# Optimization experiments

Measured on AMD Instinct MI355X. Metric: run time of the kernel, lower is better.

## Reference

```python
import jax, jax.numpy as jnp
import numpy as np

B, P, G, CIN, COUT, WD, K3 = 4, 32768, 64, 128, 128, 512, 27
N = B * P


def _build_kernel_map(rng):
    # random sparse occupancy per batch instance on a G^3 grid
    flat = np.stack([rng.choice(G ** 3, size=P, replace=False) for _ in range(B)])  # [B,P]
    b = np.repeat(np.arange(B), P).astype(np.int64)
    f = flat.reshape(-1).astype(np.int64)
    x = f // (G * G); y = (f // G) % G; z = f % G
    keys = b * (G ** 3) + f
    order = np.argsort(keys); skeys = keys[order]
    offsets = [(dx, dy, dz) for dx in (-1, 0, 1) for dy in (-1, 0, 1) for dz in (-1, 0, 1)]
    in_idx = np.full((K3, N), N, np.int32)   # N is a dummy (zero-feature) row
    out_idx = np.full((K3, N), N, np.int32)  # N is a dummy (discarded) output row
    for k, (dx, dy, dz) in enumerate(offsets):
        nx, ny, nz = x + dx, y + dy, z + dz
        inb = (nx >= 0) & (nx < G) & (ny >= 0) & (ny < G) & (nz >= 0) & (nz < G)
        nkey = b * (G ** 3) + (nx * G + ny) * G + nz
        pos = np.clip(np.searchsorted(skeys, nkey), 0, N - 1)
        found = inb & (skeys[pos] == nkey)
        cnt = int(found.sum())
        in_idx[k, :cnt] = order[pos[found]]
        out_idx[k, :cnt] = np.nonzero(found)[0]
    return b.astype(np.int32), in_idx, out_idx


def setup_inputs() -> dict:
    rng = np.random.default_rng(0)
    batch_idx, in_idx, out_idx = _build_kernel_map(rng)
    key = jax.random.key(0)
    k1, k2, k3, k4 = jax.random.split(key, 4)
    return {
        "x_feat": jax.random.normal(k1, (N, CIN), jnp.float32),
        "w": jax.random.normal(k2, (B, WD), jnp.float32),
        "affine_weight": jax.random.normal(k3, (CIN, WD), jnp.float32),
        "affine_bias": jnp.ones((CIN,), jnp.float32),  # bias_init=1
        "conv_weight": jax.random.normal(k4, (COUT, CIN, 3, 3, 3), jnp.float32),
        "conv_bias": jnp.zeros((COUT,), jnp.float32),
        "magnitude_ema": jnp.ones((), jnp.float32),
        "batch_idx": jnp.asarray(batch_idx),
        "in_idx": jnp.asarray(in_idx),
        "out_idx": jnp.asarray(out_idx),
    }


def reference(x_feat, w, affine_weight, affine_bias, conv_weight, conv_bias,
              magnitude_ema, batch_idx, in_idx, out_idx):
    n, cin = x_feat.shape
    cout = conv_weight.shape[0]
    # affine: FullyConnectedLayer with weight_gain = 1/sqrt(in_features), bias_init=1
    styles = w @ (affine_weight * (1.0 / np.sqrt(affine_weight.shape[1]))).T + affine_bias  # [B,Cin]
    # demodulate pre-normalization
    wn = conv_weight * jax.lax.rsqrt(jnp.mean(jnp.square(conv_weight), axis=(1, 2, 3, 4), keepdims=True))
    sn = styles * jax.lax.rsqrt(jnp.mean(jnp.square(styles)))
    sw = wn[None] * sn[:, None, :, None, None, None]              # [B,Cout,Cin,3,3,3]
    dcoefs = jax.lax.rsqrt(jnp.sum(jnp.square(sw), axis=(2, 3, 4, 5)) + 1e-8)  # [B,Cout]
    # non-fused modconv: per-point style modulation (index_select by batch column)
    xmod = x_feat * sn[batch_idx]                                 # [N,Cin]
    xpad = jnp.concatenate([xmod, jnp.zeros((1, cin), xmod.dtype)], axis=0)
    # sparse conv: gather -> GEMM -> scatter-add per kernel offset
    wk = jnp.transpose(wn.reshape(cout, cin, K3), (2, 1, 0))      # [27,Cin,Cout]
    out = jnp.zeros((n + 1, cout), x_feat.dtype)
    for k in range(K3):
        out = out.at[out_idx[k]].add(xpad[in_idx[k]] @ wk[k])
    out = out[:n]
    out = out * dcoefs[batch_idx]                                 # demodulation per point
    out = out * jax.lax.rsqrt(magnitude_ema)                      # input_gain
    # fused bias + leaky relu + gain + clamp
    out = out + conv_bias
    out = jnp.where(out < 0, 0.2 * out, out) * np.sqrt(2.0)
    return jnp.clip(out, -256.0, 256.0)
```

## Files before the change

### kernel.cpp

```cpp
#include <hip/hip_runtime.h>
#include <stdint.h>

#define NPTS 131072
#define CINC 128
#define COUTC 128
#define WDIM 512
#define K3 27

typedef float f32x4 __attribute__((ext_vector_type(4)));
typedef __bf16 bf16x8 __attribute__((ext_vector_type(8)));

#define GLOAD_LDS16(g, l) \
  __builtin_amdgcn_global_load_lds((const __attribute__((address_space(1))) void*)(g), \
                                   (__attribute__((address_space(3))) void*)(l), 16, 0, 0)

__device__ __forceinline__ unsigned short f2bf(float x){
  union { float f; uint32_t u; } v; v.f = x;
  uint32_t u = v.u;
  uint32_t r = (u + 0x7fffu + ((u >> 16) & 1u)) >> 16;
  return (unsigned short)r;
}

__global__ void k_styles_dot(const float* __restrict__ w, const float* __restrict__ aw,
                             const float* __restrict__ ab, float* __restrict__ styles){
  int wave = threadIdx.x >> 6, lane = threadIdx.x & 63;
  int blk = blockIdx.x * 4 + wave;
  int b = blk >> 7, c = blk & 127;
  const float4* wr = (const float4*)(w + b * WDIM);
  const float4* ar = (const float4*)(aw + c * WDIM);
  float4 w0 = wr[lane * 2], w1 = wr[lane * 2 + 1];
  float4 a0 = ar[lane * 2], a1 = ar[lane * 2 + 1];
  float s = w0.x * a0.x + w0.y * a0.y + w0.z * a0.z + w0.w * a0.w
          + w1.x * a1.x + w1.y * a1.y + w1.z * a1.z + w1.w * a1.w;
  for (int off = 32; off > 0; off >>= 1) s += __shfl_down(s, off, 64);
  if (lane == 0) styles[blk] = s * 0.04419417382415922f + ab[c];
}

__global__ void k_sn_dco(const float* __restrict__ styles, const float* __restrict__ vmat,
                         const float* __restrict__ wnorm, const float* __restrict__ mag,
                         float* __restrict__ sn, float* __restrict__ dco2){
  __shared__ float red[512];
  int t = threadIdx.x;
  float s = styles[t];
  red[t] = s * s;
  __syncthreads();
  for (int off = 256; off > 0; off >>= 1){
    if (t < off) red[t] += red[t + off];
    __syncthreads();
  }
  float rs = rsqrtf(red[0] * (1.0f / 512.0f));
  if (blockIdx.x == 0) sn[t] = s * rs;
  int wave = t >> 6, lane = t & 63;
  int pair = blockIdx.x * 8 + wave;
  int b = pair >> 7, co = pair & 127;
  float s0 = styles[b * 128 + lane] * rs, s1 = styles[b * 128 + 64 + lane] * rs;
  float sum = vmat[co * 128 + lane] * s0 * s0 + vmat[co * 128 + 64 + lane] * s1 * s1;
  for (int off = 32; off > 0; off >>= 1) sum += __shfl_down(sum, off, 64);
  if (lane == 0){
    float wn = wnorm[co];
    dco2[pair] = rsqrtf(sum * wn * wn + 1e-8f) * rsqrtf(mag[0]);
  }
}

__global__ void k_prep_w(const float* __restrict__ cw, float* __restrict__ wnorm,
                         float* __restrict__ vmat, unsigned short* __restrict__ bpack){
  __shared__ float red[128];
  int co = blockIdx.x, cin = threadIdx.x;
  const float* p = cw + co * 3456 + cin * 27;
  float r[27];
  float v = 0.f;
  #pragma unroll
  for (int k = 0; k < 27; k++){ r[k] = p[k]; v += r[k] * r[k]; }
  vmat[co * 128 + cin] = v;
  red[cin] = v;
  __syncthreads();
  for (int off = 64; off > 0; off >>= 1){
    if (cin < off) red[cin] += red[cin + off];
    __syncthreads();
  }
  float wn_s = rsqrtf(red[0] * (1.0f / 3456.0f));
  if (cin == 0) wnorm[co] = wn_s;
  int grp = co >> 4, m = co & 15;
  int kk = cin >> 5, q = (cin >> 3) & 3, j = cin & 7;
  #pragma unroll
  for (int k = 0; k < 27; k++){
    int idx = ((k * 32 + kk * 8 + grp) * 64 + q * 16 + m) * 8 + j;
    bpack[idx] = f2bf(r[k] * wn_s);
  }
}

__global__ void k_xmod(const float* __restrict__ x, const float* __restrict__ sn,
                       const int* __restrict__ bidx, unsigned short* __restrict__ xpad){
  int gid = blockIdx.x * 256 + threadIdx.x;
  const int total = (NPTS + 1) * 32;
  if (gid >= total) return;
  int n = gid >> 5;
  int c4 = (gid & 31) * 4;
  unsigned short o0, o1, o2, o3;
  if (n < NPTS){
    int b = bidx[n];
    float4 xv = *(const float4*)(x + (size_t)n * CINC + c4);
    float4 sv = *(const float4*)(sn + b * CINC + c4);
    o0 = f2bf(xv.x * sv.x); o1 = f2bf(xv.y * sv.y);
    o2 = f2bf(xv.z * sv.z); o3 = f2bf(xv.w * sv.w);
  } else { o0 = o1 = o2 = o3 = 0; }
  *(ushort4*)(xpad + (size_t)n * CINC + c4) = make_ushort4(o0, o1, o2, o3);
}

__global__ void k_invinit(int* __restrict__ invT){
  int j = blockIdx.x * 256 + threadIdx.x;
  int k = blockIdx.y;
  invT[k * NPTS + j] = NPTS;
}

__global__ void k_invscat(const int* __restrict__ out_idx, const int* __restrict__ in_idx,
                          int* __restrict__ invT){
  int j = blockIdx.x * 256 + threadIdx.x;
  int k = blockIdx.y;
  int o = out_idx[k * NPTS + j];
  if (o < NPTS) invT[k * NPTS + o] = in_idx[k * NPTS + j];
}

__global__ __launch_bounds__(256, 4) void k_conv(
    const unsigned short* __restrict__ xpad,
    const unsigned short* __restrict__ bpack,
    const int* __restrict__ invT,
    const float* __restrict__ dco2,
    const float* __restrict__ cbias,
    const int* __restrict__ bidx,
    float* __restrict__ out){
  __shared__ __align__(16) unsigned short Ash[2 * 64 * 128];
  int t = threadIdx.x;
  int wave = t >> 6, lane = t & 63;
  int wm = wave >> 1, wn = wave & 1;
  int q = lane >> 4, m16 = lane & 15;
  int base_pt = blockIdx.x * 64;

  f32x4 acc[2][4];
  #pragma unroll
  for (int i = 0; i < 2; i++)
    #pragma unroll
    for (int j = 0; j < 4; j++) acc[i][j] = (f32x4){0.f, 0.f, 0.f, 0.f};

  auto prefetch = [&](int k, int bufsel){
    const int* invk = invT + k * NPTS + base_pt;
    unsigned short* Ab = Ash + bufsel * (64 * 128);
    #pragma unroll
    for (int i = 0; i < 4; i++){
      int chunk = i * 256 + t;
      int row = chunk >> 4, c = chunk & 15;
      int inv = invk[row];
      const unsigned short* src = xpad + (size_t)inv * CINC + ((c ^ row) & 15) * 8;
      GLOAD_LDS16(src, Ab + chunk * 8);
    }
  };

  prefetch(0, 0);
  for (int k = 0; k < K3; k++){
    __syncthreads();
    if (k + 1 < K3) prefetch(k + 1, (k + 1) & 1);
    const unsigned short* Ab = Ash + (k & 1) * (64 * 128);
    const unsigned short* Bg = bpack + k * 16384;
    #pragma unroll
    for (int kk = 0; kk < 4; kk++){
      int cA = ((kk * 4 + q) ^ m16) & 15;
      bf16x8 a0 = *(const bf16x8*)(Ab + (wm * 32 + m16) * 128 + cA * 8);
      bf16x8 a1 = *(const bf16x8*)(Ab + (wm * 32 + 16 + m16) * 128 + cA * 8);
      #pragma unroll
      for (int jn = 0; jn < 4; jn++){
        bf16x8 b = *(const bf16x8*)(Bg + ((kk * 8 + wn * 4 + jn) * 64 + lane) * 8);
        acc[0][jn] = __builtin_amdgcn_mfma_f32_16x16x32_bf16(a0, b, acc[0][jn], 0, 0, 0);
        acc[1][jn] = __builtin_amdgcn_mfma_f32_16x16x32_bf16(a1, b, acc[1][jn], 0, 0, 0);
      }
    }
  }

  const float S2 = 1.41421356237309515f;
  #pragma unroll
  for (int i = 0; i < 2; i++){
    #pragma unroll
    for (int r = 0; r < 4; r++){
      int row = wm * 32 + i * 16 + q * 4 + r;
      int n = base_pt + row;
      int b = bidx[n];
      const float* dc = dco2 + b * COUTC;
      float* orow = out + (size_t)n * COUTC;
      #pragma unroll
      for (int jn = 0; jn < 4; jn++){
        int col = wn * 64 + jn * 16 + m16;
        float v = acc[i][jn][r] * dc[col] + cbias[col];
        v = (v < 0.f ? 0.2f * v : v) * S2;
        v = fminf(fmaxf(v, -256.f), 256.f);
        orow[col] = v;
      }
    }
  }
}

extern "C" void kernel_launch(void* const* d_in, const int* in_sizes, int n_in,
                              void* d_out, int out_size, void* d_ws, size_t ws_size,
                              hipStream_t stream){
  const float* x   = (const float*)d_in[0];
  const float* w   = (const float*)d_in[1];
  const float* aw  = (const float*)d_in[2];
  const float* ab  = (const float*)d_in[3];
  const float* cw  = (const float*)d_in[4];
  const float* cb  = (const float*)d_in[5];
  const float* mag = (const float*)d_in[6];
  const int* bidx    = (const int*)d_in[7];
  const int* in_idx  = (const int*)d_in[8];
  const int* out_idx = (const int*)d_in[9];
  float* out = (float*)d_out;
  char* ws = (char*)d_ws;

  float* styles = (float*)(ws + 0);
  float* sn     = (float*)(ws + 2048);
  float* wnorm  = (float*)(ws + 4096);
  float* dco2   = (float*)(ws + 4608);
  float* vmat   = (float*)(ws + 8192);
  unsigned short* bpack = (unsigned short*)(ws + 73728);
  unsigned short* xpad  = (unsigned short*)(ws + 958464);
  int* invT     = (int*)(ws + 34513152);

  k_prep_w<<<128, 128, 0, stream>>>(cw, wnorm, vmat, bpack);
  k_styles_dot<<<128, 256, 0, stream>>>(w, aw, ab, styles);
  k_sn_dco<<<64, 512, 0, stream>>>(styles, vmat, wnorm, mag, sn, dco2);
  k_xmod<<<16385, 256, 0, stream>>>(x, sn, bidx, xpad);
  dim3 gi(512, 27);
  k_invinit<<<gi, 256, 0, stream>>>(invT);
  k_invscat<<<gi, 256, 0, stream>>>(out_idx, in_idx, invT);
  k_conv<<<2048, 256, 0, stream>>>(xpad, bpack, invT, dco2, cb, bidx, out);
}
```

Measured before the change: 322.0 us.

## Deepen conv gather pipeline to 4 LDS buffers with explicit vmcnt waits

The conv kernel moves from a double-buffered to a quad-buffered LDS ring and prefetches the gathered A tiles two offsets ahead. Gather indices are loaded one stage earlier into registers, and the B weight fragments for each offset are loaded into registers before the barrier. Hand-placed s_waitcnt vmcnt counts and sched_barriers replace the plain __syncthreads so more memory latency can overlap with MFMA work. The cost is twice the LDS use and a lower launch_bounds occupancy target (2 instead of 4), and correctness depends on the hand-written vmcnt counts.

Result: no change. 328.3 us (+1.9%).

```diff
diff --git a/kernel.cpp b/kernel.cpp
--- a/kernel.cpp
+++ b/kernel.cpp
@@ -121,7 +121,7 @@
   if (o < NPTS) invT[k * NPTS + o] = in_idx[k * NPTS + j];
 }
 
-__global__ __launch_bounds__(256, 4) void k_conv(
+__global__ __launch_bounds__(256, 2) void k_conv(
     const unsigned short* __restrict__ xpad,
     const unsigned short* __restrict__ bpack,
     const int* __restrict__ invT,
@@ -129,12 +129,13 @@
     const float* __restrict__ cbias,
     const int* __restrict__ bidx,
     float* __restrict__ out){
-  __shared__ __align__(16) unsigned short Ash[2 * 64 * 128];
+  __shared__ __align__(16) unsigned short Ash[4 * 64 * 128];
   int t = threadIdx.x;
   int wave = t >> 6, lane = t & 63;
   int wm = wave >> 1, wn = wave & 1;
   int q = lane >> 4, m16 = lane & 15;
   int base_pt = blockIdx.x * 64;
+  int rbase = t >> 4, c = t & 15;
 
   f32x4 acc[2][4];
   #pragma unroll
@@ -142,25 +143,46 @@
     #pragma unroll
     for (int j = 0; j < 4; j++) acc[i][j] = (f32x4){0.f, 0.f, 0.f, 0.f};
 
-  auto prefetch = [&](int k, int bufsel){
+  auto loadIV = [&](int k, int* iv){
     const int* invk = invT + k * NPTS + base_pt;
-    unsigned short* Ab = Ash + bufsel * (64 * 128);
+    #pragma unroll
+    for (int i = 0; i < 4; i++) iv[i] = invk[i * 16 + rbase];
+  };
+  auto issueP = [&](int k, const int* iv){
+    unsigned short* Ab = Ash + (k & 3) * 8192;
     #pragma unroll
     for (int i = 0; i < 4; i++){
-      int chunk = i * 256 + t;
-      int row = chunk >> 4, c = chunk & 15;
-      int inv = invk[row];
-      const unsigned short* src = xpad + (size_t)inv * CINC + ((c ^ row) & 15) * 8;
-      GLOAD_LDS16(src, Ab + chunk * 8);
+      int row = i * 16 + rbase;
+      const unsigned short* src = xpad + (size_t)iv[i] * CINC + ((c ^ row) & 15) * 8;
+      GLOAD_LDS16(src, Ab + (i * 256 + t) * 8);
     }
   };
 
-  prefetch(0, 0);
+  int ivP[4], ivN[4];
+  loadIV(0, ivP); issueP(0, ivP);
+  loadIV(1, ivP); issueP(1, ivP);
+  loadIV(2, ivP);
+
   for (int k = 0; k < K3; k++){
-    __syncthreads();
-    if (k + 1 < K3) prefetch(k + 1, (k + 1) & 1);
-    const unsigned short* Ab = Ash + (k & 1) * (64 * 128);
+    bf16x8 b[4][4];
     const unsigned short* Bg = bpack + k * 16384;
+    #pragma unroll
+    for (int kk = 0; kk < 4; kk++)
+      #pragma unroll
+      for (int jn = 0; jn < 4; jn++)
+        b[kk][jn] = *(const bf16x8*)(Bg + ((kk * 8 + wn * 4 + jn) * 64 + lane) * 8);
+    __builtin_amdgcn_sched_barrier(0);
+    if (k + 2 < K3){
+      issueP(k + 2, ivP);
+      if (k + 3 < K3) loadIV(k + 3, ivN);
+    }
+    __builtin_amdgcn_sched_barrier(0);
+    if (k + 2 < K3) asm volatile("s_waitcnt vmcnt(8)" ::: "memory");
+    else            asm volatile("s_waitcnt vmcnt(0)" ::: "memory");
+    __builtin_amdgcn_sched_barrier(0);
+    __builtin_amdgcn_s_barrier();
+    __builtin_amdgcn_sched_barrier(0);
+    const unsigned short* Ab = Ash + (k & 3) * 8192;
     #pragma unroll
     for (int kk = 0; kk < 4; kk++){
       int cA = ((kk * 4 + q) ^ m16) & 15;
@@ -168,11 +190,13 @@
       bf16x8 a1 = *(const bf16x8*)(Ab + (wm * 32 + 16 + m16) * 128 + cA * 8);
       #pragma unroll
       for (int jn = 0; jn < 4; jn++){
-        bf16x8 b = *(const bf16x8*)(Bg + ((kk * 8 + wn * 4 + jn) * 64 + lane) * 8);
-        acc[0][jn] = __builtin_amdgcn_mfma_f32_16x16x32_bf16(a0, b, acc[0][jn], 0, 0, 0);
-        acc[1][jn] = __builtin_amdgcn_mfma_f32_16x16x32_bf16(a1, b, acc[1][jn], 0, 0, 0);
+        acc[0][jn] = __builtin_amdgcn_mfma_f32_16x16x32_bf16(a0, b[kk][jn], acc[0][jn], 0, 0, 0);
+        acc[1][jn] = __builtin_amdgcn_mfma_f32_16x16x32_bf16(a1, b[kk][jn], acc[1][jn], 0, 0, 0);
       }
     }
+    __builtin_amdgcn_sched_barrier(0);
+    #pragma unroll
+    for (int i = 0; i < 4; i++) ivP[i] = ivN[i];
   }
 
   const float S2 = 1.41421356237309515f;
```
